# Kernel tuning notes

Hardware: AMD Instinct MI355X
Metric: run time of the kernel (lower is better)

The kernel has to match this reference:

```python
import jax, jax.numpy as jnp
import numpy as np

TINY = 1e-9
S, V, H, W = 2, 4, 1024, 1024
PATCH, SKIP = 2, 2
C = PATCH * SKIP
PIX_PER_VIEW = 4096
NP_COARSE = PIX_PER_VIEW // (PATCH * PATCH)   # top-k on coarse grid
N_SAMPLED = NP_COARSE * PATCH * PATCH         # total fine pixels per view
ON_MASK = 0.9
AT_CENTER = 0.8
HC, WC = H // C, W // C


def setup_inputs() -> dict:
    key = jax.random.key(0)
    k1, k2, k3, k4, k5 = jax.random.split(key, 5)
    ys, xs = jnp.meshgrid(jnp.arange(H, dtype=jnp.float32),
                          jnp.arange(W, dtype=jnp.float32), indexing='ij')
    uv1 = jnp.stack([xs.reshape(-1), ys.reshape(-1)])            # (2, H*W): X then Y
    uv = jnp.broadcast_to(uv1[None, None], (S, V, 2, H * W)) + 0.0
    base = jnp.array([[1111.0, 0.0, W / 2.0, 0.0],
                      [0.0, 1111.0, H / 2.0, 0.0],
                      [0.0, 0.0, 1.0, 0.0],
                      [0.0, 0.0, 0.0, 1.0]], dtype=jnp.float32)
    intrinsics = jnp.broadcast_to(base[None], (S, 4, 4)) + 0.0
    A = jax.random.normal(k2, (S, V, 3, 3), dtype=jnp.float32)
    Q, _ = jnp.linalg.qr(A)                                       # random rotations
    t = 2.0 * jax.random.normal(k3, (S, V, 3), dtype=jnp.float32)
    ext = jnp.zeros((S, V, 4, 4), dtype=jnp.float32)
    ext = ext.at[..., :3, :3].set(Q).at[..., :3, 3].set(t).at[..., 3, 3].set(1.0)
    alpha = jax.random.normal(k4, (S, V, H, W), dtype=jnp.float32)
    size = jnp.stack([jnp.full((S, V), H, jnp.int32),
                      jnp.full((S, V), W, jnp.int32)], axis=-1)
    gumbel_u = jax.random.uniform(k5, (S, V, HC * WC), dtype=jnp.float32)
    full_index = jax.random.randint(k1, (S, V), 0, SKIP * SKIP)
    return dict(uv=uv, intrinsics=intrinsics, extrinsics=ext, alpha=alpha,
                size=size, gumbel_u=gumbel_u, full_index=full_index)


def _sample_pixels(uv, alpha, gumbel_u, full_index):
    # mask from alpha, restricted to image center (sampling_at_center=0.8)
    mask = (alpha > 0).astype(jnp.float32)                        # (S,V,H,W)
    r = (1.0 - AT_CENTER) / 2.0
    rh, rw = int(H * r), int(W * r)
    row_ok = (jnp.arange(H) >= rh) & (jnp.arange(H) < H - rh)
    col_ok = (jnp.arange(W) >= rw) & (jnp.arange(W) < W - rw)
    mask = mask * (row_ok[:, None] & col_ok[None, :]).astype(jnp.float32)
    probs = mask / (mask.sum() + 1e-8)                            # global normalization as in torch
    probs = ON_MASK * probs + (1.0 - ON_MASK) / (H * W)
    # pool probabilities onto the coarse (patch*skip) grid
    probs_c = probs.reshape(S, V, HC, C, WC, C).sum(axis=(3, 5))  # (S,V,HC,WC)
    logp = jnp.log(probs_c.reshape(S, V, -1) + TINY)
    g = -jnp.log(-jnp.log(gumbel_u + TINY) + TINY)                # gumbel noise
    idx = jax.lax.top_k(logp + g, NP_COARSE)[1]                   # (S,V,NP_COARSE)
    sm = jnp.zeros((S, V, HC * WC), jnp.float32)
    sm = sm.at[jnp.arange(S)[:, None, None], jnp.arange(V)[None, :, None], idx].set(1.0)
    sm = sm.reshape(S, V, HC, WC)
    # expand each coarse cell into a patch x patch block -> (S,V,H//SKIP,W//SKIP)
    sm = jnp.broadcast_to(sm[:, :, :, None, :, None],
                          (S, V, HC, PATCH, WC, PATCH)).reshape(S, V, H // SKIP, W // SKIP)
    # scatter into a random skip-slot per view, then interleave skip grid
    oh = jax.nn.one_hot(full_index, SKIP * SKIP, dtype=jnp.float32)  # (S,V,SKIP*SKIP)
    full = oh[:, :, :, None, None] * sm[:, :, None, :, :]
    sm = full.reshape(S, V, SKIP, SKIP, H // SKIP, W // SKIP)
    sm = sm.transpose(0, 1, 4, 2, 5, 3).reshape(S, V, H, W)
    # row-major gather of sampled pixels (matches torch boolean-mask gather)
    mflat = sm.reshape(S, V, H * W)
    order = jnp.argsort(-mflat, axis=-1)[..., :N_SAMPLED]         # stable: ones in row-major order
    Xs = jnp.take_along_axis(uv[:, :, 0], order, axis=-1).reshape(S, V, 1, -1, PATCH, PATCH)
    Ys = jnp.take_along_axis(uv[:, :, 1], order, axis=-1).reshape(S, V, 1, -1, PATCH, PATCH)
    return jnp.concatenate([Xs, Ys], axis=2)                      # (S,V,2,NPatch,PATCH,PATCH)


def _rays(uv_s, intrinsics, extrinsics):
    fuv = uv_s.reshape(S, V, 2, -1)                               # (S,V,2,N)
    ray_start = extrinsics[:, :, :3, 3]                           # (S,V,3)
    fx = intrinsics[:, 0, 0][:, None, None]
    fy = intrinsics[:, 1, 1][:, None, None]
    cx = intrinsics[:, 0, 2][:, None, None]
    cy = intrinsics[:, 1, 2][:, None, None]
    x = (fuv[:, :, 0] - cx) / fx                                  # z = 1 lift
    y = (fuv[:, :, 1] - cy) / fy
    ones = jnp.ones_like(x)
    cam = jnp.stack([x, y, ones, ones], axis=2)                   # (S,V,4,N) homogeneous
    world = jnp.einsum('svij,svjn->svin', extrinsics, cam)[:, :, :3]
    d = world - ray_start[..., None]
    d = d / jnp.maximum(jnp.linalg.norm(d, axis=2, keepdims=True), 1e-12)
    return ray_start[:, :, None, :], d.transpose(0, 1, 3, 2)      # (S,V,1,3), (S,V,N,3)


def reference(uv, intrinsics, extrinsics, alpha, size, gumbel_u, full_index):
    uv_s = _sample_pixels(uv, alpha, gumbel_u, full_index)
    ray_start, ray_dir = _rays(uv_s, intrinsics, extrinsics)
    return ray_start, ray_dir, uv_s
```

## Files before the change

### kernel.cpp

```cpp
#include <hip/hip_runtime.h>
#include <math.h>

#define S_ 2
#define V_ 4
#define H_ 1024
#define W_ 1024
#define NCELL 65536
#define NSV 8
#define KSEL 1024
#define CROP_LO 102
#define CROP_HI 922
#define NPIX (H_*W_)

#define NB1 32768
#define NB2 131072
#define HIST_U4 ((NB1 + NB2) * NSV / 4)

#define OFF_SEL   64
#define OFF_CNT   4096
#define OFF_PIX   4096
#define OFF_ROW   135168
#define OFF_KEYS  528384
#define OFF_H1    2625536
#define OFF_H2    3674112

static __device__ __forceinline__ unsigned score_key(float score){
  unsigned ub = __float_as_uint(score);
  return (ub & 0x80000000u) ? ~ub : (ub | 0x80000000u);
}

__global__ __launch_bounds__(64) void k_init(unsigned* __restrict__ total){
  if (threadIdx.x == 0) *total = 0u;
}

__global__ __launch_bounds__(256) void k_count(const float* __restrict__ alpha,
                                               unsigned char* __restrict__ cnt,
                                               unsigned* __restrict__ total){
  int g = blockIdx.x * 256 + threadIdx.x;
  int sv = g >> 16;
  int cell = g & (NCELL - 1);
  int hc = cell >> 8;
  int wc = cell & 255;
  const float4* ap = reinterpret_cast<const float4*>(alpha);
  int c = 0;
  int x0 = wc * 4;
#pragma unroll
  for (int dy = 0; dy < 4; ++dy){
    int y = hc * 4 + dy;
    float4 a = ap[(size_t)(sv * H_ + y) * (W_ / 4) + wc];
    if (y >= CROP_LO && y < CROP_HI){
      c += (a.x > 0.0f) & (x0 + 0 >= CROP_LO) & (x0 + 0 < CROP_HI);
      c += (a.y > 0.0f) & (x0 + 1 >= CROP_LO) & (x0 + 1 < CROP_HI);
      c += (a.z > 0.0f) & (x0 + 2 >= CROP_LO) & (x0 + 2 < CROP_HI);
      c += (a.w > 0.0f) & (x0 + 3 >= CROP_LO) & (x0 + 3 < CROP_HI);
    }
  }
  cnt[g] = (unsigned char)c;
  __shared__ unsigned red[256];
  red[threadIdx.x] = (unsigned)c;
  __syncthreads();
  for (int off = 128; off > 0; off >>= 1){
    if (threadIdx.x < off) red[threadIdx.x] += red[threadIdx.x + off];
    __syncthreads();
  }
  if (threadIdx.x == 0) atomicAdd(total, red[0]);
}

__global__ __launch_bounds__(256) void k_score(const unsigned char* __restrict__ cnt,
                                               const float* __restrict__ gum,
                                               const unsigned* __restrict__ total,
                                               unsigned* __restrict__ keys,
                                               uint4* __restrict__ histz){
  int g = blockIdx.x * 256 + threadIdx.x;
  if (g < HIST_U4) histz[g] = make_uint4(0u, 0u, 0u, 0u);
  float T = (float)(*total);
  float denom = __fadd_rn(T, 1e-8f);
  float inv = __fdiv_rn(1.0f, denom);
  const float COFF = (float)((1.0 - 0.9) / (1024.0 * 1024.0));
  float q_on = __fadd_rn(__fmul_rn(0.9f, inv), COFF);
  int k = cnt[g];
  float pc = __fadd_rn(__fmul_rn((float)k, q_on), __fmul_rn((float)(16 - k), COFF));
  float logp = logf(__fadd_rn(pc, 1e-9f));
  float u = gum[g];
  float gl = logf(__fadd_rn(u, 1e-9f));
  float gmb = -logf(__fadd_rn(-gl, 1e-9f));
  keys[g] = score_key(__fadd_rn(logp, gmb));
}

__global__ __launch_bounds__(256) void k_hist1(const unsigned* __restrict__ keys,
                                               unsigned* __restrict__ hist1){
  int sv = blockIdx.x >> 5;
  int chunk = blockIdx.x & 31;
  __shared__ unsigned h[NB1 / 2];
  for (int i = threadIdx.x; i < NB1 / 2; i += 256) h[i] = 0u;
  __syncthreads();
  const uint4* kp = reinterpret_cast<const uint4*>(keys + sv * NCELL + chunk * 2048);
#pragma unroll
  for (int i = 0; i < 2; ++i){
    uint4 k4 = kp[threadIdx.x + i * 256];
    unsigned b;
    b = k4.x >> 17; atomicAdd(&h[b >> 1], 1u << ((b & 1u) << 4));
    b = k4.y >> 17; atomicAdd(&h[b >> 1], 1u << ((b & 1u) << 4));
    b = k4.z >> 17; atomicAdd(&h[b >> 1], 1u << ((b & 1u) << 4));
    b = k4.w >> 17; atomicAdd(&h[b >> 1], 1u << ((b & 1u) << 4));
  }
  __syncthreads();
  unsigned* hb = hist1 + sv * NB1;
  for (int i = threadIdx.x; i < NB1 / 2; i += 256){
    unsigned w = h[i];
    unsigned lo = w & 0xFFFFu, hi = w >> 16;
    if (lo) atomicAdd(&hb[2 * i + 0], lo);
    if (hi) atomicAdd(&hb[2 * i + 1], hi);
  }
}

__global__ __launch_bounds__(1024) void k_pick1(const unsigned* __restrict__ hist1,
                                                unsigned* __restrict__ sel){
  const int sv = blockIdx.x;
  const int t = threadIdx.x;
  const unsigned* h = hist1 + sv * NB1;
  const unsigned target = KSEL;
  const uint4* h4 = reinterpret_cast<const uint4*>(h + t * 32);
  unsigned csum = 0;
#pragma unroll
  for (int i = 0; i < 8; ++i){
    uint4 v = h4[i];
    csum += v.x + v.y + v.z + v.w;
  }
  __shared__ unsigned sh[1024];
  sh[t] = csum;
  __syncthreads();
  for (int off = 1; off < 1024; off <<= 1){
    unsigned v = (t + off < 1024) ? sh[t + off] : 0u;
    __syncthreads();
    sh[t] += v;
    __syncthreads();
  }
  unsigned sufAbove = sh[t] - csum;
  if (sufAbove < target && sh[t] >= target){
    unsigned cum = sufAbove;
    for (int b = 31; b >= 0; --b){
      unsigned hv = h[t * 32 + b];
      cum += hv;
      if (cum >= target){
        sel[sv * 4 + 0] = (unsigned)(t * 32 + b);
        sel[sv * 4 + 1] = target - (cum - hv);
        break;
      }
    }
  }
}

__global__ __launch_bounds__(256) void k_hist2(const unsigned* __restrict__ keys,
                                               const unsigned* __restrict__ sel,
                                               unsigned* __restrict__ hist2){
  int sv = blockIdx.x >> 5;
  int chunk = blockIdx.x & 31;
  unsigned p15 = sel[sv * 4 + 0];
  const uint4* kp = reinterpret_cast<const uint4*>(keys + sv * NCELL + chunk * 2048);
  unsigned* hb = hist2 + sv * NB2;
#pragma unroll
  for (int i = 0; i < 2; ++i){
    uint4 k4 = kp[threadIdx.x + i * 256];
    if ((k4.x >> 17) == p15) atomicAdd(&hb[k4.x & 0x1FFFFu], 1u);
    if ((k4.y >> 17) == p15) atomicAdd(&hb[k4.y & 0x1FFFFu], 1u);
    if ((k4.z >> 17) == p15) atomicAdd(&hb[k4.z & 0x1FFFFu], 1u);
    if ((k4.w >> 17) == p15) atomicAdd(&hb[k4.w & 0x1FFFFu], 1u);
  }
}

__global__ __launch_bounds__(1024) void k_pick2(const unsigned* __restrict__ hist2,
                                                unsigned* __restrict__ sel){
  const int sv = blockIdx.x;
  const int t = threadIdx.x;
  const unsigned* h = hist2 + sv * NB2;
  const unsigned p15 = sel[sv * 4 + 0];
  const unsigned target = sel[sv * 4 + 1];
  const uint4* h4 = reinterpret_cast<const uint4*>(h + t * 128);
  unsigned csum = 0;
  for (int i = 0; i < 32; ++i){
    uint4 v = h4[i];
    csum += v.x + v.y + v.z + v.w;
  }
  __shared__ unsigned sh[1024];
  sh[t] = csum;
  __syncthreads();
  for (int off = 1; off < 1024; off <<= 1){
    unsigned v = (t + off < 1024) ? sh[t + off] : 0u;
    __syncthreads();
    sh[t] += v;
    __syncthreads();
  }
  unsigned sufAbove = sh[t] - csum;
  if (sufAbove < target && sh[t] >= target){
    unsigned cum = sufAbove;
    for (int b = 127; b >= 0; --b){
      unsigned hv = h[t * 128 + b];
      cum += hv;
      if (cum >= target){
        sel[sv * 4 + 2] = (p15 << 17) | (unsigned)(t * 128 + b);
        sel[sv * 4 + 3] = target - (cum - hv);
        break;
      }
    }
  }
}

__global__ __launch_bounds__(256) void k_rowcnt(const unsigned* __restrict__ keys,
                                                const unsigned* __restrict__ sel,
                                                unsigned* __restrict__ rowcnt){
  int gw = blockIdx.x * 4 + (threadIdx.x >> 6);
  int lane = threadIdx.x & 63;
  int sv = gw >> 8;
  int row = gw & 255;
  const unsigned thr = sel[sv * 4 + 2];
  uint4 k4 = *reinterpret_cast<const uint4*>(keys + sv * NCELL + row * 256 + lane * 4);
  unsigned gt = (k4.x > thr) + (k4.y > thr) + (k4.z > thr) + (k4.w > thr);
  unsigned eq = (k4.x == thr) + (k4.y == thr) + (k4.z == thr) + (k4.w == thr);
  unsigned p = (gt << 16) | eq;
#pragma unroll
  for (int off = 1; off < 64; off <<= 1) p += __shfl_xor(p, off, 64);
  if (lane == 0) rowcnt[gw] = p;
}

static __device__ __forceinline__ unsigned block_excl_scan256(unsigned v, unsigned* lds4, int t){
  int lane = t & 63, w = t >> 6;
  unsigned x = v;
#pragma unroll
  for (int off = 1; off < 64; off <<= 1){
    unsigned y = __shfl_up(x, (unsigned)off, 64);
    if (lane >= off) x += y;
  }
  if (lane == 63) lds4[w] = x;
  __syncthreads();
  unsigned base = 0;
  for (int i = 0; i < w; ++i) base += lds4[i];
  __syncthreads();
  return base + x - v;
}

__global__ __launch_bounds__(256) void k_emit2(const unsigned* __restrict__ keys,
                                               const unsigned* __restrict__ sel,
                                               const unsigned* __restrict__ rowcnt,
                                               const int* __restrict__ fidx,
                                               unsigned* __restrict__ pix){
  const int sv = blockIdx.x >> 6;
  const int t = threadIdx.x;
  __shared__ unsigned lds4[4];
  __shared__ unsigned sM[256], sP[256], sEqb[256];

  const unsigned thr = sel[sv * 4 + 2];
  const unsigned rem = sel[sv * 4 + 3];

  unsigned rc = rowcnt[sv * 256 + t];
  unsigned gt = rc >> 16, eq = rc & 0xFFFFu;
  unsigned eqbase = block_excl_scan256(eq, lds4, t);
  unsigned take_eq = 0;
  if (rem > eqbase){ take_eq = rem - eqbase; if (take_eq > eq) take_eq = eq; }
  unsigned m = gt + take_eq;
  unsigned P = block_excl_scan256(m, lds4, t);
  sM[t] = m; sP[t] = P; sEqb[t] = eqbase;
  __syncthreads();

  const int lane = t & 63;
  const int row = ((blockIdx.x & 63) << 2) + (t >> 6);
  const unsigned rm = sM[row];
  const unsigned rP = sP[row];
  const unsigned reqb = sEqb[row];

  const int fi = fidx[sv];
  const int k1 = (fi >> 1) & 1;
  const int k2 = fi & 1;
  unsigned* pb = pix + sv * 4096;

  uint4 k4 = *reinterpret_cast<const uint4*>(keys + sv * NCELL + row * 256 + lane * 4);
  unsigned kk[4] = {k4.x, k4.y, k4.z, k4.w};

  unsigned laneEq = 0;
#pragma unroll
  for (int q = 0; q < 4; ++q) laneEq += (kk[q] == thr);
  unsigned xe = laneEq;
#pragma unroll
  for (int off = 1; off < 64; off <<= 1){
    unsigned y = __shfl_up(xe, (unsigned)off, 64);
    if (lane >= off) xe += y;
  }
  unsigned eqpre = xe - laneEq;

  bool s[4];
  unsigned eqr = reqb + eqpre;
  unsigned laneSel = 0;
#pragma unroll
  for (int q = 0; q < 4; ++q){
    bool sq = (kk[q] > thr);
    if (kk[q] == thr){ if (eqr < rem) sq = true; eqr++; }
    s[q] = sq;
    laneSel += sq;
  }
  unsigned xs = laneSel;
#pragma unroll
  for (int off = 1; off < 64; off <<= 1){
    unsigned y = __shfl_up(xs, (unsigned)off, 64);
    if (lane >= off) xs += y;
  }
  unsigned jj = xs - laneSel;

  const unsigned baserank = 4u * rP;
#pragma unroll
  for (int q = 0; q < 4; ++q){
    if (!s[q]) continue;
    int wc = lane * 4 + q;
    unsigned base = baserank + 2u * jj;
    unsigned f0 = (unsigned)((4 * row + k1) * W_ + 4 * wc + k2);
    pb[base + 0]           = f0;
    pb[base + 1]           = f0 + 2u;
    pb[base + 2u * rm + 0] = f0 + 2u * W_;
    pb[base + 2u * rm + 1] = f0 + 2u * W_ + 2u;
    jj++;
  }
}

__global__ __launch_bounds__(256) void k_rays(const unsigned* __restrict__ pix,
                                              const float* __restrict__ uv,
                                              const float* __restrict__ intr,
                                              const float* __restrict__ extr,
                                              float* __restrict__ out){
  int g = blockIdx.x * 256 + threadIdx.x;
  int sv = g >> 12;
  int r = g & 4095;
  const int s = sv >> 2;
  const float fx = intr[s * 16 + 0];
  const float cx = intr[s * 16 + 2];
  const float fy = intr[s * 16 + 5];
  const float cy = intr[s * 16 + 6];
  const float e00 = extr[sv * 16 + 0], e01 = extr[sv * 16 + 1], e02 = extr[sv * 16 + 2], e03 = extr[sv * 16 + 3];
  const float e10 = extr[sv * 16 + 4], e11 = extr[sv * 16 + 5], e12 = extr[sv * 16 + 6], e13 = extr[sv * 16 + 7];
  const float e20 = extr[sv * 16 + 8], e21 = extr[sv * 16 + 9], e22 = extr[sv * 16 + 10], e23 = extr[sv * 16 + 11];
  if (r < 3) out[sv * 3 + r] = extr[sv * 16 + r * 4 + 3];

  unsigned flat = pix[g];
  const float* uvx = uv + (size_t)sv * 2 * NPIX;
  const float* uvy = uvx + NPIX;
  float X = uvx[flat];
  float Y = uvy[flat];
  float* out_dir = out + S_ * V_ * 3;
  float* out_uvs = out + S_ * V_ * 3 + S_ * V_ * 4096 * 3;
  out_uvs[(sv * 2 + 0) * 4096 + r] = X;
  out_uvs[(sv * 2 + 1) * 4096 + r] = Y;
  float xx = (X - cx) / fx;
  float yy = (Y - cy) / fy;
  float d0 = (e00 * xx + e01 * yy + e02 + e03) - e03;
  float d1 = (e10 * xx + e11 * yy + e12 + e13) - e13;
  float d2 = (e20 * xx + e21 * yy + e22 + e23) - e23;
  float nrm = sqrtf(d0 * d0 + d1 * d1 + d2 * d2);
  float den = fmaxf(nrm, 1e-12f);
  size_t ob = ((size_t)sv * 4096 + r) * 3;
  out_dir[ob + 0] = d0 / den;
  out_dir[ob + 1] = d1 / den;
  out_dir[ob + 2] = d2 / den;
}

extern "C" void kernel_launch(void* const* d_in, const int* in_sizes, int n_in,
                              void* d_out, int out_size, void* d_ws, size_t ws_size,
                              hipStream_t stream){
  (void)in_sizes; (void)n_in; (void)out_size; (void)ws_size;
  const float* uv         = (const float*)d_in[0];
  const float* intr       = (const float*)d_in[1];
  const float* extr       = (const float*)d_in[2];
  const float* alpha      = (const float*)d_in[3];
  const float* gum        = (const float*)d_in[5];
  const int*   full_index = (const int*)d_in[6];
  float* out = (float*)d_out;

  char* ws = (char*)d_ws;
  unsigned*      total  = (unsigned*)ws;
  unsigned*      sel    = (unsigned*)(ws + OFF_SEL);
  unsigned char* cnt    = (unsigned char*)(ws + OFF_CNT);
  unsigned*      pix    = (unsigned*)(ws + OFF_PIX);
  unsigned*      rowcnt = (unsigned*)(ws + OFF_ROW);
  unsigned*      keys   = (unsigned*)(ws + OFF_KEYS);
  unsigned*      hist1  = (unsigned*)(ws + OFF_H1);
  unsigned*      hist2  = (unsigned*)(ws + OFF_H2);
  uint4*         histz  = (uint4*)(ws + OFF_H1);

  hipLaunchKernelGGL(k_init,   dim3(1), dim3(64), 0, stream, total);
  hipLaunchKernelGGL(k_count,  dim3(NSV * NCELL / 256), dim3(256), 0, stream, alpha, cnt, total);
  hipLaunchKernelGGL(k_score,  dim3(NSV * NCELL / 256), dim3(256), 0, stream, cnt, gum, total, keys, histz);
  hipLaunchKernelGGL(k_hist1,  dim3(NSV * 32), dim3(256), 0, stream, keys, hist1);
  hipLaunchKernelGGL(k_pick1,  dim3(NSV), dim3(1024), 0, stream, hist1, sel);
  hipLaunchKernelGGL(k_hist2,  dim3(NSV * 32), dim3(256), 0, stream, keys, sel, hist2);
  hipLaunchKernelGGL(k_pick2,  dim3(NSV), dim3(1024), 0, stream, hist2, sel);
  hipLaunchKernelGGL(k_rowcnt, dim3(512), dim3(256), 0, stream, keys, sel, rowcnt);
  hipLaunchKernelGGL(k_emit2,  dim3(512), dim3(256), 0, stream, keys, sel, rowcnt, full_index, pix);
  hipLaunchKernelGGL(k_rays,   dim3(NSV * 4096 / 256), dim3(256), 0, stream, pix, uv, intr, extr, out);
}
```

Before: 94.47 us.

## Replace two-pass radix select with coarse histogram plus candidate compaction and rank search

```diff
diff --git a/kernel.cpp b/kernel.cpp
--- a/kernel.cpp
+++ b/kernel.cpp
@@ -12,17 +12,18 @@
 #define CROP_HI 922
 #define NPIX (H_*W_)
 
-#define NB1 32768
-#define NB2 131072
-#define HIST_U4 ((NB1 + NB2) * NSV / 4)
+#define NB1 4096
+#define NREP 4
+#define HIST_U4 (NSV * NREP * NB1 / 4)
 
 #define OFF_SEL   64
+#define OFF_CCNT  256
 #define OFF_CNT   4096
 #define OFF_PIX   4096
 #define OFF_ROW   135168
 #define OFF_KEYS  528384
 #define OFF_H1    2625536
-#define OFF_H2    3674112
+#define OFF_LIST  3674112
 
 static __device__ __forceinline__ unsigned score_key(float score){
   unsigned ub = __float_as_uint(score);
@@ -35,8 +36,10 @@
 
 __global__ __launch_bounds__(256) void k_count(const float* __restrict__ alpha,
                                                unsigned char* __restrict__ cnt,
-                                               unsigned* __restrict__ total){
+                                               unsigned* __restrict__ total,
+                                               uint4* __restrict__ histz){
   int g = blockIdx.x * 256 + threadIdx.x;
+  if (g < HIST_U4) histz[g] = make_uint4(0u, 0u, 0u, 0u);
   int sv = g >> 16;
   int cell = g & (NCELL - 1);
   int hc = cell >> 8;
@@ -69,10 +72,8 @@
 __global__ __launch_bounds__(256) void k_score(const unsigned char* __restrict__ cnt,
                                                const float* __restrict__ gum,
                                                const unsigned* __restrict__ total,
-                                               unsigned* __restrict__ keys,
-                                               uint4* __restrict__ histz){
+                                               unsigned* __restrict__ keys){
   int g = blockIdx.x * 256 + threadIdx.x;
-  if (g < HIST_U4) histz[g] = make_uint4(0u, 0u, 0u, 0u);
   float T = (float)(*total);
   float denom = __fadd_rn(T, 1e-8f);
   float inv = __fdiv_rn(1.0f, denom);
@@ -91,26 +92,23 @@
                                                unsigned* __restrict__ hist1){
   int sv = blockIdx.x >> 5;
   int chunk = blockIdx.x & 31;
-  __shared__ unsigned h[NB1 / 2];
-  for (int i = threadIdx.x; i < NB1 / 2; i += 256) h[i] = 0u;
+  __shared__ unsigned h[NB1];
+  for (int i = threadIdx.x; i < NB1; i += 256) h[i] = 0u;
   __syncthreads();
   const uint4* kp = reinterpret_cast<const uint4*>(keys + sv * NCELL + chunk * 2048);
 #pragma unroll
   for (int i = 0; i < 2; ++i){
     uint4 k4 = kp[threadIdx.x + i * 256];
-    unsigned b;
-    b = k4.x >> 17; atomicAdd(&h[b >> 1], 1u << ((b & 1u) << 4));
-    b = k4.y >> 17; atomicAdd(&h[b >> 1], 1u << ((b & 1u) << 4));
-    b = k4.z >> 17; atomicAdd(&h[b >> 1], 1u << ((b & 1u) << 4));
-    b = k4.w >> 17; atomicAdd(&h[b >> 1], 1u << ((b & 1u) << 4));
-  }
-  __syncthreads();
-  unsigned* hb = hist1 + sv * NB1;
-  for (int i = threadIdx.x; i < NB1 / 2; i += 256){
-    unsigned w = h[i];
-    unsigned lo = w & 0xFFFFu, hi = w >> 16;
-    if (lo) atomicAdd(&hb[2 * i + 0], lo);
-    if (hi) atomicAdd(&hb[2 * i + 1], hi);
+    atomicAdd(&h[k4.x >> 20], 1u);
+    atomicAdd(&h[k4.y >> 20], 1u);
+    atomicAdd(&h[k4.z >> 20], 1u);
+    atomicAdd(&h[k4.w >> 20], 1u);
+  }
+  __syncthreads();
+  unsigned* hb = hist1 + (sv * NREP + (chunk & (NREP - 1))) * NB1;
+  for (int i = threadIdx.x; i < NB1; i += 256){
+    unsigned v = h[i];
+    if (v) atomicAdd(&hb[i], v);
   }
 }
 
@@ -118,15 +116,14 @@
                                                 unsigned* __restrict__ sel){
   const int sv = blockIdx.x;
   const int t = threadIdx.x;
-  const unsigned* h = hist1 + sv * NB1;
   const unsigned target = KSEL;
-  const uint4* h4 = reinterpret_cast<const uint4*>(h + t * 32);
-  unsigned csum = 0;
-#pragma unroll
-  for (int i = 0; i < 8; ++i){
-    uint4 v = h4[i];
-    csum += v.x + v.y + v.z + v.w;
-  }
+  uint4 b4 = make_uint4(0u, 0u, 0u, 0u);
+#pragma unroll
+  for (int rep = 0; rep < NREP; ++rep){
+    uint4 v = reinterpret_cast<const uint4*>(hist1 + (sv * NREP + rep) * NB1)[t];
+    b4.x += v.x; b4.y += v.y; b4.z += v.z; b4.w += v.w;
+  }
+  unsigned csum = b4.x + b4.y + b4.z + b4.w;
   __shared__ unsigned sh[1024];
   sh[t] = csum;
   __syncthreads();
@@ -138,12 +135,13 @@
   }
   unsigned sufAbove = sh[t] - csum;
   if (sufAbove < target && sh[t] >= target){
+    unsigned bb[4] = {b4.x, b4.y, b4.z, b4.w};
     unsigned cum = sufAbove;
-    for (int b = 31; b >= 0; --b){
-      unsigned hv = h[t * 32 + b];
+    for (int b = 3; b >= 0; --b){
+      unsigned hv = bb[b];
       cum += hv;
       if (cum >= target){
-        sel[sv * 4 + 0] = (unsigned)(t * 32 + b);
+        sel[sv * 4 + 0] = (unsigned)(t * 4 + b);
         sel[sv * 4 + 1] = target - (cum - hv);
         break;
       }
@@ -151,57 +149,74 @@
   }
 }
 
-__global__ __launch_bounds__(256) void k_hist2(const unsigned* __restrict__ keys,
-                                               const unsigned* __restrict__ sel,
-                                               unsigned* __restrict__ hist2){
+__global__ __launch_bounds__(256) void k_compact(const unsigned* __restrict__ keys,
+                                                 const unsigned* __restrict__ sel,
+                                                 unsigned* __restrict__ list,
+                                                 unsigned* __restrict__ chunkcnt){
   int sv = blockIdx.x >> 5;
   int chunk = blockIdx.x & 31;
-  unsigned p15 = sel[sv * 4 + 0];
+  unsigned p12 = sel[sv * 4 + 0];
+  __shared__ unsigned lcnt;
+  if (threadIdx.x == 0) lcnt = 0u;
+  __syncthreads();
   const uint4* kp = reinterpret_cast<const uint4*>(keys + sv * NCELL + chunk * 2048);
-  unsigned* hb = hist2 + sv * NB2;
+  unsigned* seg = list + (sv * 32 + chunk) * 2048;
 #pragma unroll
   for (int i = 0; i < 2; ++i){
     uint4 k4 = kp[threadIdx.x + i * 256];
-    if ((k4.x >> 17) == p15) atomicAdd(&hb[k4.x & 0x1FFFFu], 1u);
-    if ((k4.y >> 17) == p15) atomicAdd(&hb[k4.y & 0x1FFFFu], 1u);
-    if ((k4.z >> 17) == p15) atomicAdd(&hb[k4.z & 0x1FFFFu], 1u);
-    if ((k4.w >> 17) == p15) atomicAdd(&hb[k4.w & 0x1FFFFu], 1u);
-  }
-}
-
-__global__ __launch_bounds__(1024) void k_pick2(const unsigned* __restrict__ hist2,
-                                                unsigned* __restrict__ sel){
+    unsigned kk[4] = {k4.x, k4.y, k4.z, k4.w};
+#pragma unroll
+    for (int q = 0; q < 4; ++q){
+      if ((kk[q] >> 20) == p12) seg[atomicAdd(&lcnt, 1u)] = kk[q];
+    }
+  }
+  __syncthreads();
+  if (threadIdx.x == 0) chunkcnt[sv * 32 + chunk] = lcnt;
+}
+
+__global__ __launch_bounds__(1024) void k_pick2b(const unsigned* __restrict__ list,
+                                                 const unsigned* __restrict__ chunkcnt,
+                                                 unsigned* __restrict__ sel){
   const int sv = blockIdx.x;
   const int t = threadIdx.x;
-  const unsigned* h = hist2 + sv * NB2;
-  const unsigned p15 = sel[sv * 4 + 0];
-  const unsigned target = sel[sv * 4 + 1];
-  const uint4* h4 = reinterpret_cast<const uint4*>(h + t * 128);
-  unsigned csum = 0;
-  for (int i = 0; i < 32; ++i){
-    uint4 v = h4[i];
-    csum += v.x + v.y + v.z + v.w;
-  }
-  __shared__ unsigned sh[1024];
-  sh[t] = csum;
-  __syncthreads();
-  for (int off = 1; off < 1024; off <<= 1){
-    unsigned v = (t + off < 1024) ? sh[t + off] : 0u;
-    __syncthreads();
-    sh[t] += v;
-    __syncthreads();
-  }
-  unsigned sufAbove = sh[t] - csum;
-  if (sufAbove < target && sh[t] >= target){
-    unsigned cum = sufAbove;
-    for (int b = 127; b >= 0; --b){
-      unsigned hv = h[t * 128 + b];
-      cum += hv;
-      if (cum >= target){
-        sel[sv * 4 + 2] = (p15 << 17) | (unsigned)(t * 128 + b);
-        sel[sv * 4 + 3] = target - (cum - hv);
-        break;
+  __shared__ unsigned pfx[33];
+  __shared__ unsigned seg[2048];
+  if (t == 0){
+    unsigned a = 0;
+    for (int c = 0; c < 32; ++c){ pfx[c] = a; a += chunkcnt[sv * 32 + c]; }
+    pfx[32] = a;
+  }
+  __syncthreads();
+  const unsigned n = pfx[32];
+  const unsigned rem1 = sel[sv * 4 + 1];
+  const unsigned nbatch = (n + 1023u) / 1024u;
+  for (unsigned b = 0; b < nbatch; ++b){
+    unsigned i = b * 1024u + (unsigned)t;
+    unsigned vi = 0u;
+    bool valid = (i < n);
+    if (valid){
+      int c = 0;
+      while (c < 31 && pfx[c + 1] <= i) ++c;
+      vi = list[(sv * 32 + c) * 2048 + (i - pfx[c])];
+    }
+    unsigned cgt = 0, ceq = 0;
+    for (int jc = 0; jc < 32; ++jc){
+      unsigned mj = pfx[jc + 1] - pfx[jc];
+      const unsigned* gseg = list + (sv * 32 + jc) * 2048;
+      for (unsigned j = t; j < mj; j += 1024) seg[j] = gseg[j];
+      __syncthreads();
+      if (valid){
+        for (unsigned j = 0; j < mj; ++j){
+          unsigned w = seg[j];
+          cgt += (w > vi);
+          ceq += (w == vi);
+        }
       }
+      __syncthreads();
+    }
+    if (valid && cgt < rem1 && rem1 <= cgt + ceq){
+      sel[sv * 4 + 2] = vi;
+      sel[sv * 4 + 3] = rem1 - cgt;
     }
   }
 }
@@ -373,24 +388,25 @@
   float* out = (float*)d_out;
 
   char* ws = (char*)d_ws;
-  unsigned*      total  = (unsigned*)ws;
-  unsigned*      sel    = (unsigned*)(ws + OFF_SEL);
-  unsigned char* cnt    = (unsigned char*)(ws + OFF_CNT);
-  unsigned*      pix    = (unsigned*)(ws + OFF_PIX);
-  unsigned*      rowcnt = (unsigned*)(ws + OFF_ROW);
-  unsigned*      keys   = (unsigned*)(ws + OFF_KEYS);
-  unsigned*      hist1  = (unsigned*)(ws + OFF_H1);
-  unsigned*      hist2  = (unsigned*)(ws + OFF_H2);
-  uint4*         histz  = (uint4*)(ws + OFF_H1);
-
-  hipLaunchKernelGGL(k_init,   dim3(1), dim3(64), 0, stream, total);
-  hipLaunchKernelGGL(k_count,  dim3(NSV * NCELL / 256), dim3(256), 0, stream, alpha, cnt, total);
-  hipLaunchKernelGGL(k_score,  dim3(NSV * NCELL / 256), dim3(256), 0, stream, cnt, gum, total, keys, histz);
-  hipLaunchKernelGGL(k_hist1,  dim3(NSV * 32), dim3(256), 0, stream, keys, hist1);
-  hipLaunchKernelGGL(k_pick1,  dim3(NSV), dim3(1024), 0, stream, hist1, sel);
-  hipLaunchKernelGGL(k_hist2,  dim3(NSV * 32), dim3(256), 0, stream, keys, sel, hist2);
-  hipLaunchKernelGGL(k_pick2,  dim3(NSV), dim3(1024), 0, stream, hist2, sel);
-  hipLaunchKernelGGL(k_rowcnt, dim3(512), dim3(256), 0, stream, keys, sel, rowcnt);
-  hipLaunchKernelGGL(k_emit2,  dim3(512), dim3(256), 0, stream, keys, sel, rowcnt, full_index, pix);
-  hipLaunchKernelGGL(k_rays,   dim3(NSV * 4096 / 256), dim3(256), 0, stream, pix, uv, intr, extr, out);
-}
+  unsigned*      total    = (unsigned*)ws;
+  unsigned*      sel      = (unsigned*)(ws + OFF_SEL);
+  unsigned*      chunkcnt = (unsigned*)(ws + OFF_CCNT);
+  unsigned char* cnt      = (unsigned char*)(ws + OFF_CNT);
+  unsigned*      pix      = (unsigned*)(ws + OFF_PIX);
+  unsigned*      rowcnt   = (unsigned*)(ws + OFF_ROW);
+  unsigned*      keys     = (unsigned*)(ws + OFF_KEYS);
+  unsigned*      hist1    = (unsigned*)(ws + OFF_H1);
+  uint4*         histz4   = (uint4*)(ws + OFF_H1);
+  unsigned*      list     = (unsigned*)(ws + OFF_LIST);
+
+  hipLaunchKernelGGL(k_init,    dim3(1), dim3(64), 0, stream, total);
+  hipLaunchKernelGGL(k_count,   dim3(NSV * NCELL / 256), dim3(256), 0, stream, alpha, cnt, total, histz4);
+  hipLaunchKernelGGL(k_score,   dim3(NSV * NCELL / 256), dim3(256), 0, stream, cnt, gum, total, keys);
+  hipLaunchKernelGGL(k_hist1,   dim3(NSV * 32), dim3(256), 0, stream, keys, hist1);
+  hipLaunchKernelGGL(k_pick1,   dim3(NSV), dim3(1024), 0, stream, hist1, sel);
+  hipLaunchKernelGGL(k_compact, dim3(NSV * 32), dim3(256), 0, stream, keys, sel, list, chunkcnt);
+  hipLaunchKernelGGL(k_pick2b,  dim3(NSV), dim3(1024), 0, stream, list, chunkcnt, sel);
+  hipLaunchKernelGGL(k_rowcnt,  dim3(512), dim3(256), 0, stream, keys, sel, rowcnt);
+  hipLaunchKernelGGL(k_emit2,   dim3(512), dim3(256), 0, stream, keys, sel, rowcnt, full_index, pix);
+  hipLaunchKernelGGL(k_rays,    dim3(NSV * 4096 / 256), dim3(256), 0, stream, pix, uv, intr, extr, out);
+}
```

Result: slower. 159.3 us (+68.6%).

## Split second-pass radix pick into parallel segment sums plus small refine kernel

Applied to the files above, without the earlier changes.

```diff
diff --git a/kernel.cpp b/kernel.cpp
--- a/kernel.cpp
+++ b/kernel.cpp
@@ -14,15 +14,17 @@
 
 #define NB1 32768
 #define NB2 131072
+#define NSEG 128
 #define HIST_U4 ((NB1 + NB2) * NSV / 4)
 
 #define OFF_SEL   64
-#define OFF_CNT   4096
-#define OFF_PIX   4096
-#define OFF_ROW   135168
-#define OFF_KEYS  528384
-#define OFF_H1    2625536
-#define OFF_H2    3674112
+#define OFF_SEG   256
+#define OFF_CNT   4352
+#define OFF_PIX   4352
+#define OFF_ROW   135424
+#define OFF_KEYS  528640
+#define OFF_H1    2625792
+#define OFF_H2    3674368
 
 static __device__ __forceinline__ unsigned score_key(float score){
   unsigned ub = __float_as_uint(score);
@@ -169,37 +171,65 @@
   }
 }
 
-__global__ __launch_bounds__(1024) void k_pick2(const unsigned* __restrict__ hist2,
+__global__ __launch_bounds__(256) void k_seg2(const unsigned* __restrict__ hist2,
+                                              unsigned* __restrict__ segsum){
+  int sv = blockIdx.x >> 7;
+  int seg = blockIdx.x & (NSEG - 1);
+  const uint4* h4 = reinterpret_cast<const uint4*>(hist2 + sv * NB2 + seg * 1024);
+  uint4 v = h4[threadIdx.x];
+  unsigned csum = v.x + v.y + v.z + v.w;
+  __shared__ unsigned red[256];
+  red[threadIdx.x] = csum;
+  __syncthreads();
+  for (int off = 128; off > 0; off >>= 1){
+    if (threadIdx.x < off) red[threadIdx.x] += red[threadIdx.x + off];
+    __syncthreads();
+  }
+  if (threadIdx.x == 0) segsum[sv * NSEG + seg] = red[0];
+}
+
+__global__ __launch_bounds__(256) void k_pick2c(const unsigned* __restrict__ hist2,
+                                                const unsigned* __restrict__ segsum,
                                                 unsigned* __restrict__ sel){
   const int sv = blockIdx.x;
   const int t = threadIdx.x;
-  const unsigned* h = hist2 + sv * NB2;
-  const unsigned p15 = sel[sv * 4 + 0];
-  const unsigned target = sel[sv * 4 + 1];
-  const uint4* h4 = reinterpret_cast<const uint4*>(h + t * 128);
-  unsigned csum = 0;
-  for (int i = 0; i < 32; ++i){
-    uint4 v = h4[i];
-    csum += v.x + v.y + v.z + v.w;
-  }
-  __shared__ unsigned sh[1024];
+  __shared__ unsigned ss[NSEG];
+  __shared__ int swin;
+  __shared__ unsigned stgt;
+  if (t < NSEG) ss[t] = segsum[sv * NSEG + t];
+  __syncthreads();
+  if (t == 0){
+    unsigned target = sel[sv * 4 + 1];
+    unsigned cum = 0;
+    for (int s = NSEG - 1; s >= 0; --s){
+      cum += ss[s];
+      if (cum >= target){ swin = s; stgt = target - (cum - ss[s]); break; }
+    }
+  }
+  __syncthreads();
+  const int s = swin;
+  const unsigned t2 = stgt;
+  const uint4* h4 = reinterpret_cast<const uint4*>(hist2 + sv * NB2 + s * 1024);
+  uint4 v = h4[t];
+  unsigned csum = v.x + v.y + v.z + v.w;
+  __shared__ unsigned sh[256];
   sh[t] = csum;
   __syncthreads();
-  for (int off = 1; off < 1024; off <<= 1){
-    unsigned v = (t + off < 1024) ? sh[t + off] : 0u;
-    __syncthreads();
-    sh[t] += v;
+  for (int off = 1; off < 256; off <<= 1){
+    unsigned y = (t + off < 256) ? sh[t + off] : 0u;
+    __syncthreads();
+    sh[t] += y;
     __syncthreads();
   }
   unsigned sufAbove = sh[t] - csum;
-  if (sufAbove < target && sh[t] >= target){
+  if (sufAbove < t2 && sh[t] >= t2){
+    unsigned bb[4] = {v.x, v.y, v.z, v.w};
     unsigned cum = sufAbove;
-    for (int b = 127; b >= 0; --b){
-      unsigned hv = h[t * 128 + b];
-      cum += hv;
-      if (cum >= target){
-        sel[sv * 4 + 2] = (p15 << 17) | (unsigned)(t * 128 + b);
-        sel[sv * 4 + 3] = target - (cum - hv);
+    for (int b = 3; b >= 0; --b){
+      cum += bb[b];
+      if (cum >= t2){
+        sel[sv * 4 + 2] = (sel[sv * 4 + 0] << 17) | (unsigned)(s * 1024 + t * 4 + b);
+        sel[sv * 4 + 3] = t2 - (cum - bb[b]);
         break;
       }
     }
@@ -375,6 +405,7 @@
   char* ws = (char*)d_ws;
   unsigned*      total  = (unsigned*)ws;
   unsigned*      sel    = (unsigned*)(ws + OFF_SEL);
+  unsigned*      segsum = (unsigned*)(ws + OFF_SEG);
   unsigned char* cnt    = (unsigned char*)(ws + OFF_CNT);
   unsigned*      pix    = (unsigned*)(ws + OFF_PIX);
   unsigned*      rowcnt = (unsigned*)(ws + OFF_ROW);
@@ -389,7 +420,8 @@
   hipLaunchKernelGGL(k_hist1,  dim3(NSV * 32), dim3(256), 0, stream, keys, hist1);
   hipLaunchKernelGGL(k_pick1,  dim3(NSV), dim3(1024), 0, stream, hist1, sel);
   hipLaunchKernelGGL(k_hist2,  dim3(NSV * 32), dim3(256), 0, stream, keys, sel, hist2);
-  hipLaunchKernelGGL(k_pick2,  dim3(NSV), dim3(1024), 0, stream, hist2, sel);
+  hipLaunchKernelGGL(k_seg2,   dim3(NSV * NSEG), dim3(256), 0, stream, hist2, segsum);
+  hipLaunchKernelGGL(k_pick2c, dim3(NSV), dim3(256), 0, stream, hist2, segsum, sel);
   hipLaunchKernelGGL(k_rowcnt, dim3(512), dim3(256), 0, stream, keys, sel, rowcnt);
   hipLaunchKernelGGL(k_emit2,  dim3(512), dim3(256), 0, stream, keys, sel, rowcnt, full_index, pix);
   hipLaunchKernelGGL(k_rays,   dim3(NSV * 4096 / 256), dim3(256), 0, stream, pix, uv, intr, extr, out);
```

After: 77.16 us, median of 2. -18.3%, faster.
